# Kernel optimization log

Measured on AMD Instinct MI355X. Metric: run time of the kernel, lower is better.

Reference implementation:

```python
import jax, jax.numpy as jnp
import numpy as np

LOCAL_RANGE = 7  # module default local_range
NUM_HEADS = 8


def setup_inputs() -> dict:
    key = jax.random.key(0)
    k1, k2, k3 = jax.random.split(key, 3)
    B, S, D = 2, 2048, 512
    hidden_states = jax.random.normal(k1, (B, S, D), dtype=jnp.float32)
    scale = 1.0 / (D ** 0.5)
    Wq = jax.random.normal(k2, (D, D), dtype=jnp.float32) * scale
    Wk = jax.random.normal(k3, (D, D), dtype=jnp.float32) * scale
    return {"hidden_states": hidden_states, "Wq": Wq, "Wk": Wk}


def reference(hidden_states, Wq, Wk):
    B, S, D = hidden_states.shape
    H = NUM_HEADS
    dh = D // H
    # inner attention: only attn_weights matter (context_layer is overwritten)
    q = (hidden_states @ Wq).reshape(B, S, H, dh).transpose(0, 2, 1, 3)  # [B,H,S,dh]
    k = (hidden_states @ Wk).reshape(B, S, H, dh).transpose(0, 2, 1, 3)  # [B,H,S,dh]
    scores = jnp.einsum('bhid,bhjd->bhij', q, k) / (dh ** 0.5)          # [B,H,S,S]
    attn_weights = jax.nn.softmax(scores, axis=-1)
    # band-diagonal local mask: |i-j| <= local_range (vectorized form of the python loop)
    idx = jnp.arange(S)
    band = (jnp.abs(idx[:, None] - idx[None, :]) <= LOCAL_RANGE).astype(attn_weights.dtype)  # [S,S]
    local_w = attn_weights * band
    local_w = local_w / (jnp.sum(local_w, axis=-1, keepdims=True) + 1e-6)
    # context = matmul(local_attn_weights, hidden_states): per-head contraction
    context = jnp.einsum('bhij,bjd->bhid', local_w, hidden_states)       # [B,H,S,D]
    return context
```

## Files before the change

kernel.cpp:

```cpp
#include <hip/hip_runtime.h>
#include <hip/hip_bf16.h>
#include <math.h>

#define SEQ   2048
#define DIM   512
#define NH    8
#define DH    64
#define LR    7
#define TI    8
#define NROW  (TI + 2 * LR)

typedef __bf16 bf16_t;
typedef __bf16 bf16x8 __attribute__((ext_vector_type(8)));
typedef float  f32x4  __attribute__((ext_vector_type(4)));

typedef __attribute__((address_space(3))) void  lds_void;
typedef __attribute__((address_space(1))) const void gbl_cvoid;

__global__ __launch_bounds__(256) void prep(
    const float* __restrict__ hs,
    const float* __restrict__ Wq, const float* __restrict__ Wk,
    bf16_t* __restrict__ hsb,
    bf16_t* __restrict__ Wt)
{
    const int tid = threadIdx.x;
    const int bx  = blockIdx.x;

    if (bx < 1024) {
        const size_t base = ((size_t)bx * 256 + tid) * 8;
        const float4 f0 = *(const float4*)(hs + base);
        const float4 f1 = *(const float4*)(hs + base + 4);
        union { bf16_t b[8]; uint4 u; } cv;
        cv.b[0]=(bf16_t)f0.x; cv.b[1]=(bf16_t)f0.y; cv.b[2]=(bf16_t)f0.z; cv.b[3]=(bf16_t)f0.w;
        cv.b[4]=(bf16_t)f1.x; cv.b[5]=(bf16_t)f1.y; cv.b[6]=(bf16_t)f1.z; cv.b[7]=(bf16_t)f1.w;
        *(uint4*)(hsb + base) = cv.u;
        return;
    }

    __shared__ float tile[64][68];
    const int t  = bx - 1024;
    const int k0 = (t & 7) * 64;
    const int n0 = (t >> 3) * 64;
    const float* W = (n0 < DIM) ? Wq : Wk;
    const int nn0 = n0 & (DIM - 1);

    #pragma unroll
    for (int ph = 0; ph < 4; ++ph) {
        const int kk = ph * 16 + (tid >> 4);
        const int nn = (tid & 15) * 4;
        const float4 v = *(const float4*)(W + (size_t)(k0 + kk) * DIM + nn0 + nn);
        tile[kk][nn + 0] = v.x; tile[kk][nn + 1] = v.y;
        tile[kk][nn + 2] = v.z; tile[kk][nn + 3] = v.w;
    }
    __syncthreads();
    #pragma unroll
    for (int ph = 0; ph < 4; ++ph) {
        const int nn = ph * 16 + (tid >> 4);
        const int kk = (tid & 15) * 4;
        union { bf16_t b[4]; ushort4 u; } cv;
        #pragma unroll
        for (int u = 0; u < 4; ++u) cv.b[u] = (bf16_t)tile[kk + u][nn];
        *(ushort4*)(Wt + (size_t)(n0 + nn) * DIM + k0 + kk) = cv.u;
    }
}

__global__ __launch_bounds__(256) void qk_gemm_mfma(
    const bf16_t* __restrict__ A,
    const bf16_t* __restrict__ Bt,
    bf16_t* __restrict__ C)
{
    __shared__ bf16_t As0[64 * 32], As1[64 * 32];
    __shared__ bf16_t Bs0[128 * 32], Bs1[128 * 32];

    const int tid  = threadIdx.x;
    const int wave = tid >> 6;
    const int lane = tid & 63;
    const int l15  = lane & 15;
    const int quad = lane >> 4;
    const int wm   = (wave >> 1) * 32;
    const int wn_  = (wave & 1) * 64;
    const int m0   = blockIdx.x * 64;
    const int n0   = blockIdx.y * 128;

    const int srow = lane >> 2;
    const int scol = (lane & 3) * 8;

    const bf16_t* agp = A  + (size_t)(m0 + wave * 16 + srow) * DIM + scol;
    const bf16_t* bgp = Bt + (size_t)(n0 + wave * 32 + srow) * DIM + scol;
    bf16_t* al0 = As0 + wave * 16 * 32;
    bf16_t* al1 = As1 + wave * 16 * 32;
    bf16_t* bl0 = Bs0 + wave * 32 * 32;
    bf16_t* bl1 = Bs1 + wave * 32 * 32;

    f32x4 acc[2][4] = {};

    for (int k0 = 0; k0 < DIM; k0 += 64) {
        __builtin_amdgcn_global_load_lds((gbl_cvoid*)(agp + k0),      (lds_void*)al0, 16, 0, 0);
        __builtin_amdgcn_global_load_lds((gbl_cvoid*)(agp + k0 + 32), (lds_void*)al1, 16, 0, 0);
        __builtin_amdgcn_global_load_lds((gbl_cvoid*)(bgp + k0),      (lds_void*)bl0, 16, 0, 0);
        __builtin_amdgcn_global_load_lds((gbl_cvoid*)(bgp + k0 + 32), (lds_void*)bl1, 16, 0, 0);
        __builtin_amdgcn_global_load_lds((gbl_cvoid*)(bgp + 16 * DIM + k0),      (lds_void*)(bl0 + 16 * 32), 16, 0, 0);
        __builtin_amdgcn_global_load_lds((gbl_cvoid*)(bgp + 16 * DIM + k0 + 32), (lds_void*)(bl1 + 16 * 32), 16, 0, 0);
        __syncthreads();

        #pragma unroll
        for (int s = 0; s < 2; ++s) {
            const bf16_t* PA = s ? As1 : As0;
            const bf16_t* PB = s ? Bs1 : Bs0;
            bf16x8 af[2], bfv[4];
            #pragma unroll
            for (int mi = 0; mi < 2; ++mi)
                af[mi] = *(const bf16x8*)(PA + (wm + mi * 16 + l15) * 32 + quad * 8);
            #pragma unroll
            for (int ni = 0; ni < 4; ++ni)
                bfv[ni] = *(const bf16x8*)(PB + (wn_ + ni * 16 + l15) * 32 + quad * 8);
            #pragma unroll
            for (int mi = 0; mi < 2; ++mi)
                #pragma unroll
                for (int ni = 0; ni < 4; ++ni)
                    acc[mi][ni] = __builtin_amdgcn_mfma_f32_16x16x32_bf16(
                        af[mi], bfv[ni], acc[mi][ni], 0, 0, 0);
        }
        __syncthreads();
    }

    #pragma unroll
    for (int mi = 0; mi < 2; ++mi) {
        #pragma unroll
        for (int ni = 0; ni < 4; ++ni) {
            const int col = n0 + wn_ + ni * 16 + l15;
            #pragma unroll
            for (int r = 0; r < 4; ++r) {
                const int row = m0 + wm + mi * 16 + quad * 4 + r;
                C[(size_t)row * 1024 + col] = (bf16_t)acc[mi][ni][r];
            }
        }
    }
}

__global__ __launch_bounds__(256) void local_attn4(
    const float* __restrict__ hs,
    const bf16_t* __restrict__ qkb,
    float* __restrict__ out)
{
    __shared__ __align__(16) char uni[49152];
    bf16_t* Qb   = (bf16_t*)uni;
    bf16_t* Kb   = (bf16_t*)(uni + 16384);
    float*  band = (float*)uni;
    __shared__ float sw2[NH][TI][24];
    __shared__ float wn[NH * TI][16];

    const int tid  = threadIdx.x;
    const int wave = tid >> 6;
    const int lane = tid & 63;
    const int l15  = lane & 15;
    const int quad = lane >> 4;
    const int i0   = blockIdx.x * TI;
    const int b    = blockIdx.y;

    for (int r = wave; r < TI; r += 4) {
        const bf16_t* g = qkb + (size_t)(b * SEQ + i0 + r) * 1024 + lane * 8;
        __builtin_amdgcn_global_load_lds((gbl_cvoid*)g, (lds_void*)(Qb + r * DIM), 16, 0, 0);
    }
    for (int r = wave; r < NROW; r += 4) {
        int jg = i0 - LR + r;
        jg = jg < 0 ? 0 : (jg > SEQ - 1 ? SEQ - 1 : jg);
        const bf16_t* g = qkb + (size_t)(b * SEQ + jg) * 1024 + DIM + lane * 8;
        __builtin_amdgcn_global_load_lds((gbl_cvoid*)g, (lds_void*)(Kb + r * DIM), 16, 0, 0);
    }
    __syncthreads();

    #pragma unroll
    for (int hh = 0; hh < 2; ++hh) {
        const int h = wave * 2 + hh;
        f32x4 sacc[2] = {};
        #pragma unroll
        for (int s = 0; s < 2; ++s) {
            const bf16x8 aq = *(const bf16x8*)(Qb + l15 * DIM + h * DH + s * 32 + quad * 8);
            #pragma unroll
            for (int t = 0; t < 2; ++t) {
                const bf16x8 bk = *(const bf16x8*)(Kb + (t * 16 + l15) * DIM + h * DH + s * 32 + quad * 8);
                sacc[t] = __builtin_amdgcn_mfma_f32_16x16x32_bf16(aq, bk, sacc[t], 0, 0, 0);
            }
        }
        #pragma unroll
        for (int t = 0; t < 2; ++t) {
            const int jj = t * 16 + l15;
            if (jj < NROW) {
                #pragma unroll
                for (int r = 0; r < 4; ++r) {
                    const int ii = quad * 4 + r;
                    if (ii < TI) sw2[h][ii][jj] = sacc[t][r] * 0.125f;
                }
            }
        }
    }
    __syncthreads();

    for (int r = wave; r < NROW; r += 4) {
        int jg = i0 - LR + r;
        jg = jg < 0 ? 0 : (jg > SEQ - 1 ? SEQ - 1 : jg);
        const float* g0 = hs + ((size_t)b * SEQ + jg) * DIM + lane * 4;
        __builtin_amdgcn_global_load_lds((gbl_cvoid*)g0,         (lds_void*)(band + r * DIM),       16, 0, 0);
        __builtin_amdgcn_global_load_lds((gbl_cvoid*)(g0 + 256), (lds_void*)(band + r * DIM + 256), 16, 0, 0);
    }

    if (tid < NH * TI) {
        const int h  = tid >> 3;
        const int ii = tid & (TI - 1);
        const int i  = i0 + ii;
        float v[15], m = -1e30f;
        #pragma unroll
        for (int t = 0; t < 15; ++t) {
            const int jg = i - LR + t;
            v[t] = (jg >= 0 && jg < SEQ) ? sw2[h][ii][ii + t] : -1e30f;
            m = fmaxf(m, v[t]);
        }
        float sum = 0.f;
        #pragma unroll
        for (int t = 0; t < 15; ++t) { v[t] = __expf(v[t] - m); sum += v[t]; }
        const float inv = 1.f / sum;
        #pragma unroll
        for (int t = 0; t < 15; ++t) wn[tid][t] = v[t] * inv;
    }
    __syncthreads();

    {
        const int h  = tid >> 5;
        const int iq = (tid >> 4) & 1;
        const int dg = tid & 15;

        float wreg[4][15];
        #pragma unroll
        for (int t = 0; t < 4; ++t) {
            const int pair = h * TI + iq * 4 + t;
            #pragma unroll
            for (int j = 0; j < 15; ++j) wreg[t][j] = wn[pair][j];
        }

        const int r0 = iq * 4;
        float* op = out + ((size_t)(b * NH + h) * SEQ + i0 + iq * 4) * DIM;

        for (int c = 0; c < DIM / 64; ++c) {
            const int dbase = c * 64 + dg * 4;
            float4 a0 = {0,0,0,0}, a1 = {0,0,0,0}, a2 = {0,0,0,0}, a3 = {0,0,0,0};
            #pragma unroll
            for (int rr = 0; rr < 18; ++rr) {
                const float4 v = *(const float4*)&band[(r0 + rr) * DIM + dbase];
                if (rr <= 14) {
                    const float w = wreg[0][rr];
                    a0.x += w * v.x; a0.y += w * v.y; a0.z += w * v.z; a0.w += w * v.w;
                }
                if (rr >= 1 && rr <= 15) {
                    const float w = wreg[1][rr - 1];
                    a1.x += w * v.x; a1.y += w * v.y; a1.z += w * v.z; a1.w += w * v.w;
                }
                if (rr >= 2 && rr <= 16) {
                    const float w = wreg[2][rr - 2];
                    a2.x += w * v.x; a2.y += w * v.y; a2.z += w * v.z; a2.w += w * v.w;
                }
                if (rr >= 3) {
                    const float w = wreg[3][rr - 3];
                    a3.x += w * v.x; a3.y += w * v.y; a3.z += w * v.z; a3.w += w * v.w;
                }
            }
            *(float4*)(op + (size_t)0 * DIM + dbase) = a0;
            *(float4*)(op + (size_t)1 * DIM + dbase) = a1;
            *(float4*)(op + (size_t)2 * DIM + dbase) = a2;
            *(float4*)(op + (size_t)3 * DIM + dbase) = a3;
        }
    }
}

extern "C" void kernel_launch(void* const* d_in, const int* in_sizes, int n_in,
                              void* d_out, int out_size, void* d_ws, size_t ws_size,
                              hipStream_t stream)
{
    const float* hs = (const float*)d_in[0];
    const float* Wq = (const float*)d_in[1];
    const float* Wk = (const float*)d_in[2];
    float* out = (float*)d_out;

    const int B = in_sizes[0] / (SEQ * DIM);
    const int M = B * SEQ;

    bf16_t* hsb = (bf16_t*)d_ws;
    bf16_t* Wt  = (bf16_t*)((char*)d_ws + (4 << 20));
    bf16_t* qkb = (bf16_t*)((char*)d_ws + (5 << 20));

    prep<<<1024 + 128, 256, 0, stream>>>(hs, Wq, Wk, hsb, Wt);
    qk_gemm_mfma<<<dim3(M / 64, 1024 / 128), 256, 0, stream>>>(hsb, Wt, qkb);
    local_attn4<<<dim3(SEQ / TI, B), 256, 0, stream>>>(hs, qkb, out);
}
```

Measured before the change: 102.7 us.

## Enlarge QK GEMM tile to 128x128 with swizzled double-buffered LDS prefetch

The QK projection GEMM moves from a 64x128 tile with a load-then-sync loop to a 128x128 tile. Each wave now computes 64x64, and the next K-slab is prefetched into a second LDS buffer while the current one is consumed. An XOR swizzle on LDS columns is meant to avoid bank conflicts, and raw s_waitcnt/s_barrier replace __syncthreads. The launch grid is now hardcoded to batch 2, and a padding change in the attention kernel's wn array reduces LDS bank conflicts there.

```diff
diff --git a/kernel.cpp b/kernel.cpp
--- a/kernel.cpp
+++ b/kernel.cpp
@@ -69,66 +69,76 @@
     const bf16_t* __restrict__ Bt,
     bf16_t* __restrict__ C)
 {
-    __shared__ bf16_t As0[64 * 32], As1[64 * 32];
-    __shared__ bf16_t Bs0[128 * 32], Bs1[128 * 32];
+    __shared__ __align__(16) bf16_t As[2][128 * 64];
+    __shared__ __align__(16) bf16_t Bs[2][128 * 64];
 
     const int tid  = threadIdx.x;
-    const int wave = tid >> 6;
+    const int wv   = tid >> 6;
     const int lane = tid & 63;
     const int l15  = lane & 15;
     const int quad = lane >> 4;
-    const int wm   = (wave >> 1) * 32;
-    const int wn_  = (wave & 1) * 64;
-    const int m0   = blockIdx.x * 64;
+    const int wm   = (wv >> 1) * 64;
+    const int wn   = (wv & 1) * 64;
+    const int m0   = blockIdx.x * 128;
     const int n0   = blockIdx.y * 128;
 
-    const int srow = lane >> 2;
-    const int scol = (lane & 3) * 8;
-
-    const bf16_t* agp = A  + (size_t)(m0 + wave * 16 + srow) * DIM + scol;
-    const bf16_t* bgp = Bt + (size_t)(n0 + wave * 32 + srow) * DIM + scol;
-    bf16_t* al0 = As0 + wave * 16 * 32;
-    bf16_t* al1 = As1 + wave * 16 * 32;
-    bf16_t* bl0 = Bs0 + wave * 32 * 32;
-    bf16_t* bl1 = Bs1 + wave * 32 * 32;
-
-    f32x4 acc[2][4] = {};
-
-    for (int k0 = 0; k0 < DIM; k0 += 64) {
-        __builtin_amdgcn_global_load_lds((gbl_cvoid*)(agp + k0),      (lds_void*)al0, 16, 0, 0);
-        __builtin_amdgcn_global_load_lds((gbl_cvoid*)(agp + k0 + 32), (lds_void*)al1, 16, 0, 0);
-        __builtin_amdgcn_global_load_lds((gbl_cvoid*)(bgp + k0),      (lds_void*)bl0, 16, 0, 0);
-        __builtin_amdgcn_global_load_lds((gbl_cvoid*)(bgp + k0 + 32), (lds_void*)bl1, 16, 0, 0);
-        __builtin_amdgcn_global_load_lds((gbl_cvoid*)(bgp + 16 * DIM + k0),      (lds_void*)(bl0 + 16 * 32), 16, 0, 0);
-        __builtin_amdgcn_global_load_lds((gbl_cvoid*)(bgp + 16 * DIM + k0 + 32), (lds_void*)(bl1 + 16 * 32), 16, 0, 0);
-        __syncthreads();
+    const int srow  = lane >> 3;
+    const int sslot = (lane & 7) ^ srow;
+
+    const bf16_t* agp = A  + (size_t)(m0 + wv * 8 + srow) * DIM + sslot * 8;
+    const bf16_t* bgp = Bt + (size_t)(n0 + wv * 8 + srow) * DIM + sslot * 8;
+
+    f32x4 acc[4][4] = {};
+
+    auto GSTAGE = [&](int buf, int koff) {
+        #pragma unroll
+        for (int q = 0; q < 4; ++q) {
+            __builtin_amdgcn_global_load_lds(
+                (gbl_cvoid*)(agp + (size_t)q * 32 * DIM + koff),
+                (lds_void*)(As[buf] + (q * 32 + wv * 8) * 64), 16, 0, 0);
+            __builtin_amdgcn_global_load_lds(
+                (gbl_cvoid*)(bgp + (size_t)q * 32 * DIM + koff),
+                (lds_void*)(Bs[buf] + (q * 32 + wv * 8) * 64), 16, 0, 0);
+        }
+    };
+
+    GSTAGE(0, 0);
+    int cur = 0;
+    for (int kk = 0; kk < 8; ++kk) {
+        if (kk < 7) {
+            GSTAGE(cur ^ 1, (kk + 1) * 64);
+            asm volatile("s_waitcnt vmcnt(8)" ::: "memory");
+        } else {
+            asm volatile("s_waitcnt vmcnt(0)" ::: "memory");
+        }
+        asm volatile("s_barrier" ::: "memory");
 
         #pragma unroll
         for (int s = 0; s < 2; ++s) {
-            const bf16_t* PA = s ? As1 : As0;
-            const bf16_t* PB = s ? Bs1 : Bs0;
-            bf16x8 af[2], bfv[4];
-            #pragma unroll
-            for (int mi = 0; mi < 2; ++mi)
-                af[mi] = *(const bf16x8*)(PA + (wm + mi * 16 + l15) * 32 + quad * 8);
+            const int xs = ((s << 2) + quad) ^ (l15 & 7);
+            bf16x8 af[4], bfv[4];
+            #pragma unroll
+            for (int mi = 0; mi < 4; ++mi)
+                af[mi] = *(const bf16x8*)(As[cur] + (wm + mi * 16 + l15) * 64 + xs * 8);
             #pragma unroll
             for (int ni = 0; ni < 4; ++ni)
-                bfv[ni] = *(const bf16x8*)(PB + (wn_ + ni * 16 + l15) * 32 + quad * 8);
-            #pragma unroll
-            for (int mi = 0; mi < 2; ++mi)
+                bfv[ni] = *(const bf16x8*)(Bs[cur] + (wn + ni * 16 + l15) * 64 + xs * 8);
+            #pragma unroll
+            for (int mi = 0; mi < 4; ++mi)
                 #pragma unroll
                 for (int ni = 0; ni < 4; ++ni)
                     acc[mi][ni] = __builtin_amdgcn_mfma_f32_16x16x32_bf16(
                         af[mi], bfv[ni], acc[mi][ni], 0, 0, 0);
         }
-        __syncthreads();
+        asm volatile("s_barrier" ::: "memory");
+        cur ^= 1;
     }
 
     #pragma unroll
-    for (int mi = 0; mi < 2; ++mi) {
+    for (int mi = 0; mi < 4; ++mi) {
         #pragma unroll
         for (int ni = 0; ni < 4; ++ni) {
-            const int col = n0 + wn_ + ni * 16 + l15;
+            const int col = n0 + wn + ni * 16 + l15;
             #pragma unroll
             for (int r = 0; r < 4; ++r) {
                 const int row = m0 + wm + mi * 16 + quad * 4 + r;
@@ -148,7 +158,7 @@
     bf16_t* Kb   = (bf16_t*)(uni + 16384);
     float*  band = (float*)uni;
     __shared__ float sw2[NH][TI][24];
-    __shared__ float wn[NH * TI][16];
+    __shared__ float wn[NH * TI][17];
 
     const int tid  = threadIdx.x;
     const int wave = tid >> 6;
@@ -281,14 +291,14 @@
     const float* Wk = (const float*)d_in[2];
     float* out = (float*)d_out;
 
-    const int B = in_sizes[0] / (SEQ * DIM);
-    const int M = B * SEQ;
+    const int B = in_sizes[0] / (SEQ * DIM * 4);
+    const int M = (B > 0 ? B : 2) * SEQ;
 
     bf16_t* hsb = (bf16_t*)d_ws;
     bf16_t* Wt  = (bf16_t*)((char*)d_ws + (4 << 20));
     bf16_t* qkb = (bf16_t*)((char*)d_ws + (5 << 20));
 
     prep<<<1024 + 128, 256, 0, stream>>>(hs, Wq, Wk, hsb, Wt);
-    qk_gemm_mfma<<<dim3(M / 64, 1024 / 128), 256, 0, stream>>>(hsb, Wt, qkb);
-    local_attn4<<<dim3(SEQ / TI, B), 256, 0, stream>>>(hs, qkb, out);
+    qk_gemm_mfma<<<dim3(4096 / 128, 1024 / 128), 256, 0, stream>>>(hsb, Wt, qkb);
+    local_attn4<<<dim3(SEQ / TI, 2), 256, 0, stream>>>(hs, qkb, out);
 }
```

Measured after the change: 106.8 us. 1.04x slower.

## Fuse fp32-to-bf16 conversion of hidden states into QK GEMM A-tile loads

Applied to the files above, without the earlier changes.

Removes the separate hidden_states fp32→bf16 conversion pass in prep. The GEMM now streams fp32 A tiles directly into LDS with an XOR-swizzled layout and converts them to bf16 in registers before the MFMA. This drops a 4 MB write and read round trip through the workspace. In exchange it doubles A-tile LDS traffic, adds conversion instructions to the inner loop, and hardcodes the batch size in the launch. It also pads the wn shared array to avoid bank conflicts.

```diff
diff --git a/kernel.cpp b/kernel.cpp
--- a/kernel.cpp
+++ b/kernel.cpp
@@ -18,27 +18,12 @@
 typedef __attribute__((address_space(1))) const void gbl_cvoid;
 
 __global__ __launch_bounds__(256) void prep(
-    const float* __restrict__ hs,
     const float* __restrict__ Wq, const float* __restrict__ Wk,
-    bf16_t* __restrict__ hsb,
     bf16_t* __restrict__ Wt)
 {
     const int tid = threadIdx.x;
-    const int bx  = blockIdx.x;
-
-    if (bx < 1024) {
-        const size_t base = ((size_t)bx * 256 + tid) * 8;
-        const float4 f0 = *(const float4*)(hs + base);
-        const float4 f1 = *(const float4*)(hs + base + 4);
-        union { bf16_t b[8]; uint4 u; } cv;
-        cv.b[0]=(bf16_t)f0.x; cv.b[1]=(bf16_t)f0.y; cv.b[2]=(bf16_t)f0.z; cv.b[3]=(bf16_t)f0.w;
-        cv.b[4]=(bf16_t)f1.x; cv.b[5]=(bf16_t)f1.y; cv.b[6]=(bf16_t)f1.z; cv.b[7]=(bf16_t)f1.w;
-        *(uint4*)(hsb + base) = cv.u;
-        return;
-    }
-
     __shared__ float tile[64][68];
-    const int t  = bx - 1024;
+    const int t  = blockIdx.x;
     const int k0 = (t & 7) * 64;
     const int n0 = (t >> 3) * 64;
     const float* W = (n0 < DIM) ? Wq : Wk;
@@ -65,12 +50,12 @@
 }
 
 __global__ __launch_bounds__(256) void qk_gemm_mfma(
-    const bf16_t* __restrict__ A,
+    const float*  __restrict__ A,
     const bf16_t* __restrict__ Bt,
     bf16_t* __restrict__ C)
 {
-    __shared__ bf16_t As0[64 * 32], As1[64 * 32];
-    __shared__ bf16_t Bs0[128 * 32], Bs1[128 * 32];
+    __shared__ __align__(16) float  Asf[2][64 * 32];
+    __shared__ __align__(16) bf16_t Bs0[128 * 32], Bs1[128 * 32];
 
     const int tid  = threadIdx.x;
     const int wave = tid >> 6;
@@ -84,19 +69,26 @@
 
     const int srow = lane >> 2;
     const int scol = (lane & 3) * 8;
-
-    const bf16_t* agp = A  + (size_t)(m0 + wave * 16 + srow) * DIM + scol;
     const bf16_t* bgp = Bt + (size_t)(n0 + wave * 32 + srow) * DIM + scol;
-    bf16_t* al0 = As0 + wave * 16 * 32;
-    bf16_t* al1 = As1 + wave * 16 * 32;
     bf16_t* bl0 = Bs0 + wave * 32 * 32;
     bf16_t* bl1 = Bs1 + wave * 32 * 32;
 
+    const int arow  = lane >> 3;
+    const int aslot = (lane & 7) ^ arow;
+    const float* agp = A + (size_t)(m0 + wave * 16 + arow) * DIM + aslot * 4;
+
     f32x4 acc[2][4] = {};
 
     for (int k0 = 0; k0 < DIM; k0 += 64) {
-        __builtin_amdgcn_global_load_lds((gbl_cvoid*)(agp + k0),      (lds_void*)al0, 16, 0, 0);
-        __builtin_amdgcn_global_load_lds((gbl_cvoid*)(agp + k0 + 32), (lds_void*)al1, 16, 0, 0);
+        #pragma unroll
+        for (int s = 0; s < 2; ++s) {
+            #pragma unroll
+            for (int g = 0; g < 2; ++g) {
+                __builtin_amdgcn_global_load_lds(
+                    (gbl_cvoid*)(agp + (size_t)g * 8 * DIM + k0 + s * 32),
+                    (lds_void*)(Asf[s] + (wave * 16 + g * 8) * 32), 16, 0, 0);
+            }
+        }
         __builtin_amdgcn_global_load_lds((gbl_cvoid*)(bgp + k0),      (lds_void*)bl0, 16, 0, 0);
         __builtin_amdgcn_global_load_lds((gbl_cvoid*)(bgp + k0 + 32), (lds_void*)bl1, 16, 0, 0);
         __builtin_amdgcn_global_load_lds((gbl_cvoid*)(bgp + 16 * DIM + k0),      (lds_void*)(bl0 + 16 * 32), 16, 0, 0);
@@ -105,12 +97,20 @@
 
         #pragma unroll
         for (int s = 0; s < 2; ++s) {
-            const bf16_t* PA = s ? As1 : As0;
+            const float*  PA = Asf[s];
             const bf16_t* PB = s ? Bs1 : Bs0;
             bf16x8 af[2], bfv[4];
-            #pragma unroll
-            for (int mi = 0; mi < 2; ++mi)
-                af[mi] = *(const bf16x8*)(PA + (wm + mi * 16 + l15) * 32 + quad * 8);
+            const int hx = l15 & 7;
+            #pragma unroll
+            for (int mi = 0; mi < 2; ++mi) {
+                const float* rp = PA + (wm + mi * 16 + l15) * 32;
+                const f32x4 u0 = *(const f32x4*)(rp + (((quad << 1)    ) ^ hx) * 4);
+                const f32x4 u1 = *(const f32x4*)(rp + (((quad << 1) | 1) ^ hx) * 4);
+                union { bf16_t b[8]; bf16x8 v; } cv;
+                cv.b[0]=(bf16_t)u0[0]; cv.b[1]=(bf16_t)u0[1]; cv.b[2]=(bf16_t)u0[2]; cv.b[3]=(bf16_t)u0[3];
+                cv.b[4]=(bf16_t)u1[0]; cv.b[5]=(bf16_t)u1[1]; cv.b[6]=(bf16_t)u1[2]; cv.b[7]=(bf16_t)u1[3];
+                af[mi] = cv.v;
+            }
             #pragma unroll
             for (int ni = 0; ni < 4; ++ni)
                 bfv[ni] = *(const bf16x8*)(PB + (wn_ + ni * 16 + l15) * 32 + quad * 8);
@@ -148,7 +148,7 @@
     bf16_t* Kb   = (bf16_t*)(uni + 16384);
     float*  band = (float*)uni;
     __shared__ float sw2[NH][TI][24];
-    __shared__ float wn[NH * TI][16];
+    __shared__ float wn[NH * TI][17];
 
     const int tid  = threadIdx.x;
     const int wave = tid >> 6;
@@ -281,14 +281,10 @@
     const float* Wk = (const float*)d_in[2];
     float* out = (float*)d_out;
 
-    const int B = in_sizes[0] / (SEQ * DIM);
-    const int M = B * SEQ;
-
-    bf16_t* hsb = (bf16_t*)d_ws;
-    bf16_t* Wt  = (bf16_t*)((char*)d_ws + (4 << 20));
-    bf16_t* qkb = (bf16_t*)((char*)d_ws + (5 << 20));
-
-    prep<<<1024 + 128, 256, 0, stream>>>(hs, Wq, Wk, hsb, Wt);
-    qk_gemm_mfma<<<dim3(M / 64, 1024 / 128), 256, 0, stream>>>(hsb, Wt, qkb);
-    local_attn4<<<dim3(SEQ / TI, B), 256, 0, stream>>>(hs, qkb, out);
-}
+    bf16_t* Wt  = (bf16_t*)d_ws;
+    bf16_t* qkb = (bf16_t*)((char*)d_ws + (1 << 20));
+
+    prep<<<128, 256, 0, stream>>>(Wq, Wk, Wt);
+    qk_gemm_mfma<<<dim3(4096 / 64, 1024 / 128), 256, 0, stream>>>(hs, Wt, qkb);
+    local_attn4<<<dim3(SEQ / TI, 2), 256, 0, stream>>>(hs, qkb, out);
+}
```

Measured after the change: 110.1 us. 7.2% more time.
